# Optimization experiments

Measured on AMD Instinct MI355X. Metric: run time of the kernel, lower is better.

The kernel has to match this reference:

```python
import jax, jax.numpy as jnp
import numpy as np

N, E, F, H, R, NB, G, C = 100000, 500000, 128, 64, 16, 30, 1000, 10


def setup_inputs() -> dict:
    key = jax.random.key(0)
    ks = jax.random.split(key, 12)
    s = 0.05
    x = jax.random.normal(ks[0], (N, F), jnp.float32)
    edge_index = jax.random.randint(ks[1], (2, E), 0, N, dtype=jnp.int32)
    edge_norm = jax.random.uniform(ks[2], (E,), jnp.float32)
    edge_type = jax.random.randint(ks[3], (E,), 0, R, dtype=jnp.int32)
    seq_lengths = jnp.full((G,), N // G, dtype=jnp.int32)  # 1000 graphs x 100 nodes
    return dict(
        x=x, edge_index=edge_index, edge_norm=edge_norm, edge_type=edge_type,
        seq_lengths=seq_lengths, avec=0,
        w1_rel=jax.random.normal(ks[4], (F, H), jnp.float32) * s,
        w1_root=jax.random.normal(ks[5], (F, H), jnp.float32) * s,
        b1=jnp.zeros((H,), jnp.float32),
        bases=jax.random.normal(ks[6], (NB, H, H), jnp.float32) * s,
        comp=jax.random.normal(ks[7], (R, NB), jnp.float32) * s,
        w2_root=jax.random.normal(ks[8], (H, H), jnp.float32) * s,
        b2=jnp.zeros((H,), jnp.float32),
        lin_w=jax.random.normal(ks[9], (2 * (F + H), H), jnp.float32) * s,
        lin_b=jnp.zeros((H,), jnp.float32),
        fc_w=jax.random.normal(ks[10], (H, C), jnp.float32) * s,
        fc_b=jnp.zeros((C,), jnp.float32),
    )


def reference(x, edge_index, edge_norm, edge_type, seq_lengths, avec,
              w1_rel, w1_root, b1, bases, comp, w2_root, b2,
              lin_w, lin_b, fc_w, fc_b):
    src, dst = edge_index[0], edge_index[1]

    # --- GraphConv (PyG): out_i = W_rel @ sum_{j->i} w_ji x_j + W_root x_i + b
    msg = x[src] * edge_norm[:, None]                       # [E, F]
    agg = jax.ops.segment_sum(msg, dst, num_segments=N)     # [N, F]
    h = agg @ w1_rel + x @ w1_root + b1                     # [N, H]

    # --- RGCNConv with basis decomposition, mean aggregation per relation
    W = jnp.einsum('rb,bio->rio', comp, bases)              # [R, H, H]
    hs = h[src]                                             # [E, H]
    out = h @ w2_root + b2                                  # root transform + bias
    for r in range(R):  # small fixed relation count
        m = (edge_type == r).astype(h.dtype)                # [E]
        s_r = jax.ops.segment_sum(hs * m[:, None], dst, num_segments=N)
        c_r = jax.ops.segment_sum(m, dst, num_segments=N)
        out = out + (s_r / jnp.maximum(c_r, 1.0)[:, None]) @ W[r]

    feats = jnp.concatenate([x, out], axis=-1)              # [N, F+H]

    # --- ragged per-graph sum & max pooling (replaces the Python loop)
    bounds = jnp.cumsum(seq_lengths)
    gid = jnp.searchsorted(bounds, jnp.arange(N), side='right')  # [N] graph ids
    gsum = jax.ops.segment_sum(feats, gid, num_segments=G)       # [G, F+H]
    gmax = jax.ops.segment_max(feats, gid, num_segments=G)       # [G, F+H]

    hidden = jax.nn.relu(jnp.concatenate([gsum, gmax], -1) @ lin_w + lin_b)
    # dropout is identity at inference
    logits = hidden @ fc_w + fc_b                           # [G, C]
    if avec:
        return logits
    return jax.nn.log_softmax(logits, -1)
```

## Files before the change

### kernel.cpp

```cpp
#include <hip/hip_runtime.h>
#include <hip/hip_bf16.h>

#define NN 100000
#define NE 500000
#define FD 128
#define HD 64
#define RR 16
#define NBASE 30
#define GG 1000
#define CC 10
#define NGROUP 6250
#define NBLK ((NE + 255) / 256)
#define NDBLK ((NN + 256) / 256)
#define TOTZ (NN * RR + GG * HD * 2)
#define ZBLK ((TOTZ + 1023) / 1024)


typedef __attribute__((ext_vector_type(8))) short bf16x8;
typedef __attribute__((ext_vector_type(4))) float f32x4;

__device__ inline unsigned short f2b(float x) {
  __hip_bfloat16 b = __float2bfloat16(x);
  return *reinterpret_cast<unsigned short*>(&b);
}
__device__ inline float b2f(unsigned short u) {
  return __uint_as_float(((unsigned)u) << 16);
}
__device__ inline unsigned pk2(float a, float b) {
  return (unsigned)f2b(a) | ((unsigned)f2b(b) << 16);
}
__device__ inline unsigned fkey(float f) {
  unsigned b = __float_as_uint(f);
  return (b & 0x80000000u) ? ~b : (b | 0x80000000u);
}
__device__ inline float fdec(unsigned k) {
  unsigned b = (k & 0x80000000u) ? (k & 0x7FFFFFFFu) : ~k;
  return __uint_as_float(b);
}

__global__ void k_prep(const float* comp, const float* bases, const float* w_root,
                       const float* w_rel, const float* w2, unsigned short* Wt,
                       unsigned short* wcat2, unsigned short* w2t, int* zbase) {
  int bx = blockIdx.x;
  if (bx < 256) {
    int idx = bx * 256 + threadIdx.x;
    int r = idx >> 12, kj = idx & 4095;
    int k = kj >> 6, n = kj & 63;
    float acc = 0.0f;
    for (int b = 0; b < NBASE; ++b)
      acc += comp[r * NBASE + b] * bases[b * 4096 + kj];
    int sk = (k & 15) * 4 + (k >> 4);
    Wt[(r << 12) + n * 64 + sk] = f2b(acc);
  } else if (bx < 336) {
    int idx = (bx - 256) * 256 + threadIdx.x;
    if (idx < 16384) {
      int n = idx >> 7, k = idx & 127;
      float v = (n < 64) ? w_root[k * 64 + n] : w_rel[k * 64 + (n - 64)];
      int nt = n >> 4, m = n & 15;
      int s = k >> 5, q = (k >> 3) & 3, j = k & 7;
      wcat2[(((nt * 4 + s) * 64) + q * 16 + m) * 8 + j] = f2b(v);
    } else if (idx < 16384 + 4096) {
      int i2 = idx - 16384;
      int n = i2 >> 6, k = i2 & 63;
      int sk = (k & 15) * 4 + (k >> 4);
      w2t[n * 64 + sk] = f2b(w2[k * 64 + n]);
    }
  } else {
    int idx = (bx - 336) * 1024 + threadIdx.x * 4;
    if (idx < TOTZ)
      *reinterpret_cast<int4*>(zbase + idx) = make_int4(0, 0, 0, 0);
  }
}

__global__ __launch_bounds__(256) void k_proj_mfma(const float* x, const unsigned short* wcat2,
                                                   const float* b1, unsigned short* hroot_bf,
                                                   unsigned short* xw_bf) {
  __shared__ unsigned short wsh[16384];
  int wv = threadIdx.x >> 6, l = threadIdx.x & 63, m = l & 15, q = l >> 4;
  int g = blockIdx.x * 4 + wv;
  int gc = (g < NGROUP) ? g : (NGROUP - 1);
  size_t n0 = (size_t)gc * 16;
  const float* xr = x + (n0 + m) * FD + q * 8;
  float4 xv[8];
#pragma unroll
  for (int s = 0; s < 4; ++s) {
    xv[2 * s] = *reinterpret_cast<const float4*>(xr + s * 32);
    xv[2 * s + 1] = *reinterpret_cast<const float4*>(xr + s * 32 + 4);
  }
  {
    const uint4* wsrc = reinterpret_cast<const uint4*>(wcat2);
    uint4* wdst = reinterpret_cast<uint4*>(wsh);
#pragma unroll
    for (int r = 0; r < 8; ++r)
      wdst[r * 256 + threadIdx.x] = wsrc[r * 256 + threadIdx.x];
  }
  __syncthreads();
  if (g >= NGROUP) return;
  bf16x8 afr[4];
#pragma unroll
  for (int s = 0; s < 4; ++s) {
    float4 xa = xv[2 * s], xb = xv[2 * s + 1];
    bf16x8 a;
    a[0] = (short)f2b(xa.x); a[1] = (short)f2b(xa.y);
    a[2] = (short)f2b(xa.z); a[3] = (short)f2b(xa.w);
    a[4] = (short)f2b(xb.x); a[5] = (short)f2b(xb.y);
    a[6] = (short)f2b(xb.z); a[7] = (short)f2b(xb.w);
    afr[s] = a;
  }
  f32x4 acc[8];
#pragma unroll
  for (int nt = 0; nt < 8; ++nt) acc[nt] = (f32x4){0, 0, 0, 0};
#pragma unroll
  for (int s = 0; s < 4; ++s) {
#pragma unroll
    for (int nt = 0; nt < 8; ++nt) {
      bf16x8 b = *reinterpret_cast<const bf16x8*>(wsh + (size_t)((nt * 4 + s) * 64 + l) * 8);
      acc[nt] = __builtin_amdgcn_mfma_f32_16x16x32_bf16(afr[s], b, acc[nt], 0, 0, 0);
    }
  }
  float bv[4];
#pragma unroll
  for (int nt = 0; nt < 4; ++nt) bv[nt] = b1[nt * 16 + m];
#pragma unroll
  for (int i = 0; i < 4; ++i) {
    size_t row = (n0 + q * 4 + i) * 64 + m * 4;
    uint2 oh, ox;
    oh.x = pk2(acc[0][i] + bv[0], acc[1][i] + bv[1]);
    oh.y = pk2(acc[2][i] + bv[2], acc[3][i] + bv[3]);
    ox.x = pk2(acc[4][i], acc[5][i]);
    ox.y = pk2(acc[6][i], acc[7][i]);
    *reinterpret_cast<uint2*>(hroot_bf + row) = oh;
    *reinterpret_cast<uint2*>(xw_bf + row) = ox;
  }
}

__global__ void k_hists(const int* ei, const int* etype, int* bch, int* hist2) {
  __shared__ int lh[RR];
  if (threadIdx.x < RR) lh[threadIdx.x] = 0;
  __syncthreads();
  int e = blockIdx.x * 256 + threadIdx.x;
  if (e < NE) {
    int t = etype[e];
    atomicAdd(&lh[t], 1);
    atomicAdd(&hist2[ei[NE + e] * RR + t], 1);
  }
  __syncthreads();
  if (threadIdx.x < RR) bch[blockIdx.x * RR + threadIdx.x] = lh[threadIdx.x];
}

__device__ inline int block_scan_incl(int v, int* ps, int t) {
  ps[t] = v;
  __syncthreads();
  for (int off = 1; off < 256; off <<= 1) {
    int u = (t >= off) ? ps[t - off] : 0;
    __syncthreads();
    ps[t] += u;
    __syncthreads();
  }
  return ps[t];
}

__device__ inline int dst_degree(const int* hist2, int dst) {
  const int4* hp = reinterpret_cast<const int4*>(hist2 + dst * RR);
  int4 a = hp[0], b = hp[1], c = hp[2], d = hp[3];
  return a.x + a.y + a.z + a.w + b.x + b.y + b.z + b.w +
         c.x + c.y + c.z + c.w + d.x + d.y + d.z + d.w;
}

__global__ void k_scanA(const int* hist2, int* bsum) {
  __shared__ int red[256];
  int t = threadIdx.x;
  int dst = blockIdx.x * 256 + t;
  red[t] = (dst < NN) ? dst_degree(hist2, dst) : 0;
  __syncthreads();
  for (int s = 128; s; s >>= 1) {
    if (t < s) red[t] += red[t + s];
    __syncthreads();
  }
  if (t == 0) bsum[blockIdx.x] = red[0];
}

__global__ void k_scanC(const int* hist2, const int* bsum, int* rowptr_d, int* ctr_d) {
  int t = threadIdx.x;
  int dst = blockIdx.x * 256 + t;
  int v = (dst < NN) ? dst_degree(hist2, dst) : 0;
  __shared__ int ps[256];
  int incl = block_scan_incl(v, ps, t);
  int ex = bsum[blockIdx.x] + incl - v;
  if (dst <= NN) { rowptr_d[dst] = ex; ctr_d[dst] = ex; }
}

__global__ void k_bscan(const int* bch, const int* seq, int* bsum, int* bbase,
                        int* offs, int* bounds) {
  __shared__ int part[16][17], chunkbase[16][17];
  __shared__ int colbase[16];
  __shared__ int ps[256];
  int t = threadIdx.x;
  {
    int i0 = t * 2, i1 = t * 2 + 1;
    int l0 = (i0 < NDBLK) ? bsum[i0] : 0;
    int l1 = (i1 < NDBLK) ? bsum[i1] : 0;
    int sa = l0 + l1;
    int incla = block_scan_incl(sa, ps, t);
    int run = incla - sa;
    if (i0 < NDBLK) bsum[i0] = run;
    run += l0;
    if (i1 < NDBLK) bsum[i1] = run;
  }
  __syncthreads();
  int ty = t & 15, ck = t >> 4;
  const int CH = (NBLK + 15) / 16;
  int b0 = ck * CH, b1 = min(b0 + CH, NBLK);
  int s = 0;
  for (int b = b0; b < b1; ++b) s += bch[b * 16 + ty];
  part[ck][ty] = s;
  __syncthreads();
  if (t < 16) {
    int run = 0;
    for (int c = 0; c < 16; ++c) { chunkbase[c][t] = run; run += part[c][t]; }
    colbase[t] = run;
  }
  __syncthreads();
  if (t == 0) {
    int run = 0;
    for (int r = 0; r < RR; ++r) { int v = colbase[r]; offs[r] = run; colbase[r] = run; run += v; }
    offs[RR] = run;
  }
  __syncthreads();
  {
    int run = colbase[ty] + chunkbase[ck][ty];
    for (int b = b0; b < b1; ++b) {
      int v = bch[b * 16 + ty];
      bbase[b * 16 + ty] = run;
      run += v;
    }
  }
  __syncthreads();
  int loc[4];
  int ss = 0;
  if (t < 250) {
    for (int i = 0; i < 4; ++i) { loc[i] = seq[t * 4 + i]; ss += loc[i]; }
  }
  int incl = block_scan_incl(ss, ps, t);
  int base = incl - ss;
  if (t < 250) {
    int run = base;
    for (int i = 0; i < 4; ++i) { run += loc[i]; bounds[t * 4 + i] = run; }
  }
}

__global__ void k_sort(const int* ei, const int* etype, const float* enorm,
                       const int* bbase, const int* hist2, int* ctr_d,
                       uint4* tse, uint2* esen) {
  __shared__ int lcnt[RR];
  if (threadIdx.x < RR) lcnt[threadIdx.x] = 0;
  __syncthreads();
  int e = blockIdx.x * 256 + threadIdx.x;
  if (e >= NE) return;
  int t = etype[e];
  int rank = atomicAdd(&lcnt[t], 1);
  int p = bbase[blockIdx.x * RR + t] + rank;
  int src = ei[e];
  int dst = ei[NE + e];
  int cnt = hist2[dst * RR + t];
  float inv = 1.0f / (float)max(cnt, 1);
  int pos = atomicAdd(&ctr_d[dst], 1);
  esen[pos] = make_uint2((unsigned)src, __float_as_uint(enorm[e]));
  tse[p] = make_uint4((unsigned)src, __float_as_uint(inv), (unsigned)pos, 0u);
}

__global__ __launch_bounds__(256) void k_gconv_seg(const int* rowptr_d, const uint2* esen,
    const unsigned short* xw_bf, const unsigned short* hroot_bf, unsigned short* h_bf) {
  int wv = threadIdx.x >> 6, l = threadIdx.x & 63;
  int c4 = l & 15, eq = l >> 4;
  int dst = blockIdx.x * 4 + wv;
  int lo = rowptr_d[dst];
  int hi = rowptr_d[dst + 1];
  float4 acc = {0.0f, 0.0f, 0.0f, 0.0f};
  for (int base0 = lo; base0 < hi; base0 += 64) {
    int n = min(64, hi - base0);
    int sv = 0;
    float nv = 0.0f;
    if (l < n) {
      uint2 se = esen[base0 + l];
      sv = (int)se.x;
      nv = __uint_as_float(se.y);
    }
    int k4max = (n + 3) >> 2;
    for (int k4 = 0; k4 < k4max; ++k4) {
      int eid = k4 * 4 + eq;
      int s = __shfl(sv, eid);
      float w = __shfl(nv, eid);
      if (eid < n) {
        uint2 v = *reinterpret_cast<const uint2*>(xw_bf + (size_t)s * 64 + c4 * 4);
        acc.x += b2f((unsigned short)(v.x & 0xffffu)) * w;
        acc.y += b2f((unsigned short)(v.x >> 16)) * w;
        acc.z += b2f((unsigned short)(v.y & 0xffffu)) * w;
        acc.w += b2f((unsigned short)(v.y >> 16)) * w;
      }
    }
  }
  acc.x += __shfl_xor(acc.x, 16); acc.y += __shfl_xor(acc.y, 16);
  acc.z += __shfl_xor(acc.z, 16); acc.w += __shfl_xor(acc.w, 16);
  acc.x += __shfl_xor(acc.x, 32); acc.y += __shfl_xor(acc.y, 32);
  acc.z += __shfl_xor(acc.z, 32); acc.w += __shfl_xor(acc.w, 32);
  if (l < 16) {
    uint2 hb = *reinterpret_cast<const uint2*>(hroot_bf + (size_t)dst * 64 + l * 4);
    acc.x += b2f((unsigned short)(hb.x & 0xffffu));
    acc.y += b2f((unsigned short)(hb.x >> 16));
    acc.z += b2f((unsigned short)(hb.y & 0xffffu));
    acc.w += b2f((unsigned short)(hb.y >> 16));
    uint2 o;
    o.x = pk2(acc.x, acc.y);
    o.y = pk2(acc.z, acc.w);
    *reinterpret_cast<uint2*>(h_bf + (size_t)dst * 64 + l * 4) = o;
  }
}

__global__ __launch_bounds__(256) void k_rgcn_y(const uint4* tse, const int* offs,
    const unsigned short* h_bf, const unsigned short* Wt, unsigned short* y_bf) {
  int r = blockIdx.x;
  int lo = offs[r], hi = offs[r + 1];
  int cnt = hi - lo;
  int wv = threadIdx.x >> 6;
  int l = threadIdx.x & 63;
  int m = l & 15, q = l >> 4;
  int ngroups = (cnt + 15) / 16;
  const unsigned short* Wr = Wt + (r << 12);
  bf16x8 bfr[2][4];
#pragma unroll
  for (int s = 0; s < 2; ++s)
#pragma unroll
    for (int nt = 0; nt < 4; ++nt)
      bfr[s][nt] = *reinterpret_cast<const bf16x8*>(Wr + (nt * 16 + m) * 64 + s * 32 + q * 8);

  for (int g = blockIdx.y * 4 + wv; g < ngroups; g += gridDim.y * 4) {
    int base = lo + g * 16;
    int ne = min(16, hi - base);
    int p = base + ((m < ne) ? m : 0);
    uint4 t4 = tse[p];
    int src = (int)t4.x;
    float inv = __uint_as_float(t4.y);
    int pos = (int)t4.z;
    f32x4 acc[4];
#pragma unroll
    for (int nt = 0; nt < 4; ++nt) acc[nt] = (f32x4){0, 0, 0, 0};
    const unsigned short* hrow = h_bf + (size_t)src * 64 + q * 8;
#pragma unroll
    for (int s = 0; s < 2; ++s) {
      bf16x8 afr = *reinterpret_cast<const bf16x8*>(hrow + s * 32);
#pragma unroll
      for (int nt = 0; nt < 4; ++nt)
        acc[nt] = __builtin_amdgcn_mfma_f32_16x16x32_bf16(afr, bfr[s][nt], acc[nt], 0, 0, 0);
    }
#pragma unroll
    for (int i = 0; i < 4; ++i) {
      int row = q * 4 + i;
      float ir = __shfl(inv, row);
      int pr = __shfl(pos, row);
      if (row < ne) {
        uint2 o;
        o.x = pk2(acc[0][i] * ir, acc[1][i] * ir);
        o.y = pk2(acc[2][i] * ir, acc[3][i] * ir);
        *reinterpret_cast<uint2*>(y_bf + (size_t)pr * 64 + m * 4) = o;
      }
    }
  }
}

__global__ __launch_bounds__(256) void k_out(const int* rowptr_d, const unsigned short* y_bf,
    const unsigned short* h_bf, const unsigned short* w2t, const float* b2,
    const int* bounds, float* gsum_out, unsigned* gmax_out) {
  __shared__ float ldsC[16][68];
  __shared__ int gidv[16];
  int wv = threadIdx.x >> 6, l = threadIdx.x & 63;
  int c4 = l & 15, eq = l >> 4;
  size_t d0 = (size_t)blockIdx.x * 16;
  if (threadIdx.x < 16) {
    int dst = (int)d0 + threadIdx.x;
    int lo2 = 0, hi2 = GG;
    while (lo2 < hi2) {
      int mid = (lo2 + hi2) >> 1;
      if (bounds[mid] <= dst) lo2 = mid + 1; else hi2 = mid;
    }
    gidv[threadIdx.x] = lo2;
  }
  for (int dd = 0; dd < 4; ++dd) {
    int dst = (int)d0 + wv * 4 + dd;
    int lo = rowptr_d[dst];
    int hi = rowptr_d[dst + 1];
    float4 acc = {0.0f, 0.0f, 0.0f, 0.0f};
    for (int row = lo + eq; row < hi; row += 4) {
      uint2 v = *reinterpret_cast<const uint2*>(y_bf + (size_t)row * 64 + c4 * 4);
      acc.x += b2f((unsigned short)(v.x & 0xffffu));
      acc.y += b2f((unsigned short)(v.x >> 16));
      acc.z += b2f((unsigned short)(v.y & 0xffffu));
      acc.w += b2f((unsigned short)(v.y >> 16));
    }
    acc.x += __shfl_xor(acc.x, 16); acc.y += __shfl_xor(acc.y, 16);
    acc.z += __shfl_xor(acc.z, 16); acc.w += __shfl_xor(acc.w, 16);
    acc.x += __shfl_xor(acc.x, 32); acc.y += __shfl_xor(acc.y, 32);
    acc.z += __shfl_xor(acc.z, 32); acc.w += __shfl_xor(acc.w, 32);
    if (l < 16)
      *reinterpret_cast<float4*>(&ldsC[wv * 4 + dd][l * 4]) = acc;
  }
  __syncthreads();
  int m = l & 15, q = l >> 4, nt = wv;
  float bb = b2[nt * 16 + m];
  f32x4 acc;
#pragma unroll
  for (int i = 0; i < 4; ++i) acc[i] = ldsC[q * 4 + i][m * 4 + nt] + bb;
#pragma unroll
  for (int s = 0; s < 2; ++s) {
    bf16x8 a = *reinterpret_cast<const bf16x8*>(h_bf + (d0 + m) * 64 + s * 32 + q * 8);
    bf16x8 b = *reinterpret_cast<const bf16x8*>(w2t + (nt * 16 + m) * 64 + s * 32 + q * 8);
    acc = __builtin_amdgcn_mfma_f32_16x16x32_bf16(a, b, acc, 0, 0, 0);
  }
  int c = nt * 16 + m;
  int g0 = gidv[q * 4], g3 = gidv[q * 4 + 3];
  if (g0 == g3) {
    float ssum = acc[0] + acc[1] + acc[2] + acc[3];
    float smax = fmaxf(fmaxf(acc[0], acc[1]), fmaxf(acc[2], acc[3]));
    atomicAdd(&gsum_out[g0 * 64 + c], ssum);
    atomicMax(&gmax_out[g0 * 64 + c], fkey(smax));
  } else {
#pragma unroll
    for (int i = 0; i < 4; ++i) {
      int gg = gidv[q * 4 + i];
      atomicAdd(&gsum_out[gg * 64 + c], acc[i]);
      atomicMax(&gmax_out[gg * 64 + c], fkey(acc[i]));
    }
  }
}

__global__ __launch_bounds__(256) void k_head(const float* x, const int* bounds,
    const float* gsum_out, const unsigned* gmax_out, const float* lin_w, const float* lin_b,
    const float* fc_w, const float* fc_b, float* dout) {
  __shared__ float4 psum[8][32], pmax[8][32];
  __shared__ float gsum[192], gmax[192];
  __shared__ float part[4][64];
  __shared__ float hid[HD], lg[CC], mred[2];
  int g = blockIdx.x, t = threadIdx.x;
  int lo = (g == 0) ? 0 : bounds[g - 1];
  int hi = bounds[g];
  int nn = hi - lo;
  {
    int c4 = t & 31, ch = t >> 5;
    int a = lo + (nn * ch) / 8, b = lo + (nn * (ch + 1)) / 8;
    float4 s = {0, 0, 0, 0};
    float4 mx = {-3.4e38f, -3.4e38f, -3.4e38f, -3.4e38f};
    const float* bp = x + (size_t)a * FD + c4 * 4;
    int n = a;
    for (; n + 4 <= b; n += 4) {
      float4 v0 = *reinterpret_cast<const float4*>(bp);
      float4 v1 = *reinterpret_cast<const float4*>(bp + FD);
      float4 v2 = *reinterpret_cast<const float4*>(bp + 2 * FD);
      float4 v3 = *reinterpret_cast<const float4*>(bp + 3 * FD);
      bp += 4 * FD;
      s.x += v0.x + v1.x + v2.x + v3.x;
      s.y += v0.y + v1.y + v2.y + v3.y;
      s.z += v0.z + v1.z + v2.z + v3.z;
      s.w += v0.w + v1.w + v2.w + v3.w;
      mx.x = fmaxf(fmaxf(fmaxf(mx.x, v0.x), fmaxf(v1.x, v2.x)), v3.x);
      mx.y = fmaxf(fmaxf(fmaxf(mx.y, v0.y), fmaxf(v1.y, v2.y)), v3.y);
      mx.z = fmaxf(fmaxf(fmaxf(mx.z, v0.z), fmaxf(v1.z, v2.z)), v3.z);
      mx.w = fmaxf(fmaxf(fmaxf(mx.w, v0.w), fmaxf(v1.w, v2.w)), v3.w);
    }
    for (; n < b; ++n) {
      float4 v = *reinterpret_cast<const float4*>(bp);
      bp += FD;
      s.x += v.x; s.y += v.y; s.z += v.z; s.w += v.w;
      mx.x = fmaxf(mx.x, v.x); mx.y = fmaxf(mx.y, v.y);
      mx.z = fmaxf(mx.z, v.z); mx.w = fmaxf(mx.w, v.w);
    }
    psum[ch][c4] = s;
    pmax[ch][c4] = mx;
  }
  __syncthreads();
  if (t < 32) {
    float4 s = psum[0][t], m = pmax[0][t];
#pragma unroll
    for (int ch = 1; ch < 8; ++ch) {
      float4 ps = psum[ch][t], pm = pmax[ch][t];
      s.x += ps.x; s.y += ps.y; s.z += ps.z; s.w += ps.w;
      m.x = fmaxf(m.x, pm.x); m.y = fmaxf(m.y, pm.y);
      m.z = fmaxf(m.z, pm.z); m.w = fmaxf(m.w, pm.w);
    }
    gsum[t * 4 + 0] = s.x; gsum[t * 4 + 1] = s.y;
    gsum[t * 4 + 2] = s.z; gsum[t * 4 + 3] = s.w;
    gmax[t * 4 + 0] = m.x; gmax[t * 4 + 1] = m.y;
    gmax[t * 4 + 2] = m.z; gmax[t * 4 + 3] = m.w;
  } else if (t < 96) {
    int c = t - 32;
    gsum[128 + c] = gsum_out[g * 64 + c];
    gmax[128 + c] = fdec(gmax_out[g * 64 + c]);
  }
  __syncthreads();
  {
    int o = t & 63, pp = t >> 6;
    float a = 0.0f;
    int k0 = pp * 96;
    for (int k = k0; k < k0 + 96; ++k) {
      float gv = (k < 192) ? gsum[k] : gmax[k - 192];
      a += gv * lin_w[k * 64 + o];
    }
    part[pp][o] = a;
  }
  __syncthreads();
  if (t < HD) {
    float a = lin_b[t] + part[0][t] + part[1][t] + part[2][t] + part[3][t];
    hid[t] = fmaxf(a, 0.0f);
  }
  __syncthreads();
  if (t < CC) {
    float a = fc_b[t];
    for (int k = 0; k < HD; ++k) a += hid[k] * fc_w[k * CC + t];
    lg[t] = a;
  }
  __syncthreads();
  if (t == 0) {
    float mm = lg[0];
#pragma unroll
    for (int i = 1; i < CC; ++i) mm = fmaxf(mm, lg[i]);
    float se = 0.0f;
#pragma unroll
    for (int i = 0; i < CC; ++i) se += __expf(lg[i] - mm);
    mred[0] = mm;
    mred[1] = __logf(se);
  }
  __syncthreads();
  if (t < CC) dout[g * CC + t] = lg[t] - mred[0] - mred[1];
}

extern "C" void kernel_launch(void* const* d_in, const int* in_sizes, int n_in,
                              void* d_out, int out_size, void* d_ws, size_t ws_size,
                              hipStream_t stream) {
  const float* x     = (const float*)d_in[0];
  const int* ei      = (const int*)d_in[1];
  const float* enorm = (const float*)d_in[2];
  const int* etype   = (const int*)d_in[3];
  const int* seq     = (const int*)d_in[4];
  const float* w1_rel  = (const float*)d_in[6];
  const float* w1_root = (const float*)d_in[7];
  const float* b1      = (const float*)d_in[8];
  const float* bases   = (const float*)d_in[9];
  const float* comp    = (const float*)d_in[10];
  const float* w2      = (const float*)d_in[11];
  const float* b2      = (const float*)d_in[12];
  const float* lin_w   = (const float*)d_in[13];
  const float* lin_b   = (const float*)d_in[14];
  const float* fc_w    = (const float*)d_in[15];
  const float* fc_b    = (const float*)d_in[16];
  float* dout = (float*)d_out;

  char* p = (char*)d_ws;
  unsigned short* hroot_bf = (unsigned short*)p; p += (size_t)NN * 64 * 2;
  unsigned short* xw_bf    = (unsigned short*)p; p += (size_t)NN * 64 * 2;
  unsigned short* y_bf = (unsigned short*)p; p += (size_t)NE * 64 * 2;
  unsigned short* h_bf = (unsigned short*)p; p += (size_t)NN * 64 * 2;
  unsigned short* Wt   = (unsigned short*)p; p += (size_t)RR * 4096 * 2;
  unsigned short* wcat2 = (unsigned short*)p; p += (size_t)128 * 128 * 2;
  unsigned short* w2t  = (unsigned short*)p; p += (size_t)64 * 64 * 2;
  uint4* tse   = (uint4*)p; p += (size_t)NE * 16;
  uint2* esen  = (uint2*)p; p += (size_t)NE * 8;
  int* hist2   = (int*)p; p += (size_t)NN * RR * 4;
  float* gsum_out = (float*)p; p += (size_t)GG * 64 * 4;
  unsigned* gmax_out = (unsigned*)p; p += (size_t)GG * 64 * 4;
  int* rowptr_d = (int*)p; p += (size_t)(NDBLK * 256) * 4;
  int* ctr_d   = (int*)p; p += (size_t)(NDBLK * 256) * 4;
  int* bch     = (int*)p; p += (size_t)NBLK * RR * 4;
  int* bbase   = (int*)p; p += (size_t)NBLK * RR * 4;
  int* bsum    = (int*)p; p += (size_t)NGROUP * 4;
  int* offs    = (int*)p; p += 68;
  int* bounds  = (int*)p; p += (size_t)GG * 4;

  hipLaunchKernelGGL(k_prep, dim3(336 + ZBLK), dim3(256), 0, stream,
                     comp, bases, w1_root, w1_rel, w2, Wt, wcat2, w2t, hist2);
  hipLaunchKernelGGL(k_proj_mfma, dim3((NGROUP + 3) / 4), dim3(256), 0, stream,
                     x, wcat2, b1, hroot_bf, xw_bf);
  hipLaunchKernelGGL(k_hists, dim3(NBLK), dim3(256), 0, stream, ei, etype, bch, hist2);
  hipLaunchKernelGGL(k_scanA, dim3(NDBLK), dim3(256), 0, stream, hist2, bsum);
  hipLaunchKernelGGL(k_bscan, dim3(1), dim3(256), 0, stream, bch, seq, bsum, bbase, offs, bounds);
  hipLaunchKernelGGL(k_scanC, dim3(NDBLK), dim3(256), 0, stream, hist2, bsum, rowptr_d, ctr_d);
  hipLaunchKernelGGL(k_sort, dim3(NBLK), dim3(256), 0, stream,
                     ei, etype, enorm, bbase, hist2, ctr_d, tse, esen);
  hipLaunchKernelGGL(k_gconv_seg, dim3(NN / 4), dim3(256), 0, stream,
                     rowptr_d, esen, xw_bf, hroot_bf, h_bf);
  hipLaunchKernelGGL(k_rgcn_y, dim3(RR, 128), dim3(256), 0, stream,
                     tse, offs, h_bf, Wt, y_bf);
  hipLaunchKernelGGL(k_out, dim3(NN / 16), dim3(256), 0, stream,
                     rowptr_d, y_bf, h_bf, w2t, b2, bounds, gsum_out, gmax_out);
  hipLaunchKernelGGL(k_head, dim3(GG), dim3(256), 0, stream, x, bounds,
                     gsum_out, gmax_out, lin_w, lin_b, fc_w, fc_b, dout);
}
```

Before: 350.4 us.

## Replace global atomic graph pooling with per-block partials reduced in head kernel

k_out no longer issues atomicAdd/atomicMax into per-graph buffers. Each block now reduces its 16 nodes into at most two graph segments with wave shuffles and writes them as per-block partials, which k_head combines by scanning the blocks that cover each graph. This removes the global atomics and the zero-initialisation of the pooling buffers done in k_prep. The y_bf gather is also widened to 16-byte loads with 8 rows in flight. The partial scheme assumes each 16-node block spans at most two graphs, which holds for the 100-node test graphs.

```diff
diff --git a/kernel.cpp b/kernel.cpp
--- a/kernel.cpp
+++ b/kernel.cpp
@@ -12,7 +12,8 @@
 #define NGROUP 6250
 #define NBLK ((NE + 255) / 256)
 #define NDBLK ((NN + 256) / 256)
-#define TOTZ (NN * RR + GG * HD * 2)
+#define NOBLK (NN / 16)
+#define TOTZ (NN * RR)
 #define ZBLK ((TOTZ + 1023) / 1024)
 
 
@@ -28,14 +29,6 @@
 }
 __device__ inline unsigned pk2(float a, float b) {
   return (unsigned)f2b(a) | ((unsigned)f2b(b) << 16);
-}
-__device__ inline unsigned fkey(float f) {
-  unsigned b = __float_as_uint(f);
-  return (b & 0x80000000u) ? ~b : (b | 0x80000000u);
-}
-__device__ inline float fdec(unsigned k) {
-  unsigned b = (k & 0x80000000u) ? (k & 0x7FFFFFFFu) : ~k;
-  return __uint_as_float(b);
 }
 
 __global__ void k_prep(const float* comp, const float* bases, const float* w_root,
@@ -370,11 +363,11 @@
 
 __global__ __launch_bounds__(256) void k_out(const int* rowptr_d, const unsigned short* y_bf,
     const unsigned short* h_bf, const unsigned short* w2t, const float* b2,
-    const int* bounds, float* gsum_out, unsigned* gmax_out) {
+    const int* bounds, float* psum_p, float* pmax_p) {
   __shared__ float ldsC[16][68];
   __shared__ int gidv[16];
   int wv = threadIdx.x >> 6, l = threadIdx.x & 63;
-  int c4 = l & 15, eq = l >> 4;
+  int c8 = l & 7, eq8 = l >> 3;
   size_t d0 = (size_t)blockIdx.x * 16;
   if (threadIdx.x < 16) {
     int dst = (int)d0 + threadIdx.x;
@@ -389,20 +382,30 @@
     int dst = (int)d0 + wv * 4 + dd;
     int lo = rowptr_d[dst];
     int hi = rowptr_d[dst + 1];
-    float4 acc = {0.0f, 0.0f, 0.0f, 0.0f};
-    for (int row = lo + eq; row < hi; row += 4) {
-      uint2 v = *reinterpret_cast<const uint2*>(y_bf + (size_t)row * 64 + c4 * 4);
-      acc.x += b2f((unsigned short)(v.x & 0xffffu));
-      acc.y += b2f((unsigned short)(v.x >> 16));
-      acc.z += b2f((unsigned short)(v.y & 0xffffu));
-      acc.w += b2f((unsigned short)(v.y >> 16));
-    }
-    acc.x += __shfl_xor(acc.x, 16); acc.y += __shfl_xor(acc.y, 16);
-    acc.z += __shfl_xor(acc.z, 16); acc.w += __shfl_xor(acc.w, 16);
-    acc.x += __shfl_xor(acc.x, 32); acc.y += __shfl_xor(acc.y, 32);
-    acc.z += __shfl_xor(acc.z, 32); acc.w += __shfl_xor(acc.w, 32);
-    if (l < 16)
-      *reinterpret_cast<float4*>(&ldsC[wv * 4 + dd][l * 4]) = acc;
+    float4 aA = {0.0f, 0.0f, 0.0f, 0.0f};
+    float4 aB = {0.0f, 0.0f, 0.0f, 0.0f};
+    for (int row = lo + eq8; row < hi; row += 8) {
+      uint4 v = *reinterpret_cast<const uint4*>(y_bf + (size_t)row * 64 + c8 * 8);
+      aA.x += b2f((unsigned short)(v.x & 0xffffu));
+      aA.y += b2f((unsigned short)(v.x >> 16));
+      aA.z += b2f((unsigned short)(v.y & 0xffffu));
+      aA.w += b2f((unsigned short)(v.y >> 16));
+      aB.x += b2f((unsigned short)(v.z & 0xffffu));
+      aB.y += b2f((unsigned short)(v.z >> 16));
+      aB.z += b2f((unsigned short)(v.w & 0xffffu));
+      aB.w += b2f((unsigned short)(v.w >> 16));
+    }
+#pragma unroll
+    for (int off = 8; off <= 32; off <<= 1) {
+      aA.x += __shfl_xor(aA.x, off); aA.y += __shfl_xor(aA.y, off);
+      aA.z += __shfl_xor(aA.z, off); aA.w += __shfl_xor(aA.w, off);
+      aB.x += __shfl_xor(aB.x, off); aB.y += __shfl_xor(aB.y, off);
+      aB.z += __shfl_xor(aB.z, off); aB.w += __shfl_xor(aB.w, off);
+    }
+    if (l < 8) {
+      *reinterpret_cast<float4*>(&ldsC[wv * 4 + dd][l * 8]) = aA;
+      *reinterpret_cast<float4*>(&ldsC[wv * 4 + dd][l * 8 + 4]) = aB;
+    }
   }
   __syncthreads();
   int m = l & 15, q = l >> 4, nt = wv;
@@ -417,24 +420,30 @@
     acc = __builtin_amdgcn_mfma_f32_16x16x32_bf16(a, b, acc, 0, 0, 0);
   }
   int c = nt * 16 + m;
-  int g0 = gidv[q * 4], g3 = gidv[q * 4 + 3];
-  if (g0 == g3) {
-    float ssum = acc[0] + acc[1] + acc[2] + acc[3];
-    float smax = fmaxf(fmaxf(acc[0], acc[1]), fmaxf(acc[2], acc[3]));
-    atomicAdd(&gsum_out[g0 * 64 + c], ssum);
-    atomicMax(&gmax_out[g0 * 64 + c], fkey(smax));
-  } else {
-#pragma unroll
-    for (int i = 0; i < 4; ++i) {
-      int gg = gidv[q * 4 + i];
-      atomicAdd(&gsum_out[gg * 64 + c], acc[i]);
-      atomicMax(&gmax_out[gg * 64 + c], fkey(acc[i]));
-    }
+  int gA = gidv[0];
+  float sA = 0.0f, xA = -3.4e38f, sB = 0.0f, xB = -3.4e38f;
+#pragma unroll
+  for (int i = 0; i < 4; ++i) {
+    int gi = gidv[q * 4 + i];
+    if (gi == gA) { sA += acc[i]; xA = fmaxf(xA, acc[i]); }
+    else          { sB += acc[i]; xB = fmaxf(xB, acc[i]); }
+  }
+#pragma unroll
+  for (int off = 16; off <= 32; off <<= 1) {
+    sA += __shfl_xor(sA, off); xA = fmaxf(xA, __shfl_xor(xA, off));
+    sB += __shfl_xor(sB, off); xB = fmaxf(xB, __shfl_xor(xB, off));
+  }
+  if (q == 0) {
+    size_t base = (size_t)blockIdx.x * 128;
+    psum_p[base + c] = sA;
+    psum_p[base + 64 + c] = sB;
+    pmax_p[base + c] = xA;
+    pmax_p[base + 64 + c] = xB;
   }
 }
 
 __global__ __launch_bounds__(256) void k_head(const float* x, const int* bounds,
-    const float* gsum_out, const unsigned* gmax_out, const float* lin_w, const float* lin_b,
+    const float* psum_p, const float* pmax_p, const float* lin_w, const float* lin_b,
     const float* fc_w, const float* fc_b, float* dout) {
   __shared__ float4 psum[8][32], pmax[8][32];
   __shared__ float gsum[192], gmax[192];
@@ -492,8 +501,21 @@
     gmax[t * 4 + 2] = m.z; gmax[t * 4 + 3] = m.w;
   } else if (t < 96) {
     int c = t - 32;
-    gsum[128 + c] = gsum_out[g * 64 + c];
-    gmax[128 + c] = fdec(gmax_out[g * 64 + c]);
+    int blo = lo >> 4, bhi = (hi - 1) >> 4;
+    float s = 0.0f, mx = -3.4e38f;
+    for (int b = blo; b <= bhi; ++b) {
+      size_t base = (size_t)b * 128;
+      if (b * 16 >= lo) {
+        s += psum_p[base + c];
+        mx = fmaxf(mx, pmax_p[base + c]);
+      }
+      if (b * 16 + 15 < hi) {
+        s += psum_p[base + 64 + c];
+        mx = fmaxf(mx, pmax_p[base + 64 + c]);
+      }
+    }
+    gsum[128 + c] = s;
+    gmax[128 + c] = mx;
   }
   __syncthreads();
   {
@@ -564,8 +586,8 @@
   uint4* tse   = (uint4*)p; p += (size_t)NE * 16;
   uint2* esen  = (uint2*)p; p += (size_t)NE * 8;
   int* hist2   = (int*)p; p += (size_t)NN * RR * 4;
-  float* gsum_out = (float*)p; p += (size_t)GG * 64 * 4;
-  unsigned* gmax_out = (unsigned*)p; p += (size_t)GG * 64 * 4;
+  float* psum_p = (float*)p; p += (size_t)NOBLK * 128 * 4;
+  float* pmax_p = (float*)p; p += (size_t)NOBLK * 128 * 4;
   int* rowptr_d = (int*)p; p += (size_t)(NDBLK * 256) * 4;
   int* ctr_d   = (int*)p; p += (size_t)(NDBLK * 256) * 4;
   int* bch     = (int*)p; p += (size_t)NBLK * RR * 4;
@@ -588,8 +610,8 @@
                      rowptr_d, esen, xw_bf, hroot_bf, h_bf);
   hipLaunchKernelGGL(k_rgcn_y, dim3(RR, 128), dim3(256), 0, stream,
                      tse, offs, h_bf, Wt, y_bf);
-  hipLaunchKernelGGL(k_out, dim3(NN / 16), dim3(256), 0, stream,
-                     rowptr_d, y_bf, h_bf, w2t, b2, bounds, gsum_out, gmax_out);
+  hipLaunchKernelGGL(k_out, dim3(NOBLK), dim3(256), 0, stream,
+                     rowptr_d, y_bf, h_bf, w2t, b2, bounds, psum_p, pmax_p);
   hipLaunchKernelGGL(k_head, dim3(GG), dim3(256), 0, stream, x, bounds,
-                     gsum_out, gmax_out, lin_w, lin_b, fc_w, fc_b, dout);
-}
+                     psum_p, pmax_p, lin_w, lin_b, fc_w, fc_b, dout);
+}
```

Result: faster. 338.4 us (-3.4%).
